# Kernel tuning notes

Measured on AMD Instinct MI355X. Metric: run time of the kernel, lower is better.

Reference implementation:

```python
import jax, jax.numpy as jnp
import numpy as np

R, N, B = 3, 8192, 4096
IN_DIM, HID, OUT = 256, 128, 64
EPS = 1e-5


def _bn(x, g, b):
    # BatchNorm1d in training mode: biased batch stats over dim 0
    m = jnp.mean(x, axis=0)
    v = jnp.var(x, axis=0)
    return (x - m) * jax.lax.rsqrt(v + EPS) * g + b


def setup_inputs() -> dict:
    key = jax.random.key(0)
    k1, k2, k3, k4, k5 = jax.random.split(key, 5)
    features = jax.random.normal(k1, (N, IN_DIM), dtype=jnp.float32)
    u = jax.random.uniform(k2, (R, N, N), dtype=jnp.float32)
    adj = (u < 0.01).astype(jnp.float32)
    batch_nodes = jax.random.randint(k3, (B,), 0, N, dtype=jnp.int32)
    w1 = jax.random.uniform(k4, (IN_DIM, HID), dtype=jnp.float32)  # torch.rand init
    w2 = jax.random.uniform(k5, (HID, OUT), dtype=jnp.float32)
    return {
        "features": features, "adj": adj, "batch_nodes": batch_nodes,
        "w1": w1, "w2": w2,
        "gamma1": jnp.ones((IN_DIM,), jnp.float32), "beta1": jnp.zeros((IN_DIM,), jnp.float32),
        "gamma2": jnp.ones((OUT,), jnp.float32), "beta2": jnp.zeros((OUT,), jnp.float32),
    }


def reference(features, adj, batch_nodes, w1, w2, gamma1, beta1, gamma2, beta2):
    # gather batch subgraph
    x = features[batch_nodes]                       # [B, IN_DIM]
    bA = jnp.take(jnp.take(adj, batch_nodes, axis=1), batch_nodes, axis=2)  # [R, B, B]
    xn = _bn(x, gamma1, beta1)                      # shared across relations

    def per_relation(badj):
        A = badj + jnp.eye(B, dtype=badj.dtype)
        # D_mx.inverse().sqrt() of a diagonal degree matrix == diag(deg^-1/2)
        dinv = jax.lax.rsqrt(jnp.sum(A, axis=1))    # [B]
        A_hat = A * dinv[:, None] * dinv[None, :]   # D^-1/2 A D^-1/2
        h1 = jax.nn.sigmoid(jax.nn.elu((A_hat @ xn) @ w1))   # conv1 + sigmoid
        h2 = jax.nn.elu((A_hat @ h1) @ w2)                   # conv2
        return _bn(h2, gamma2, beta2)

    embed = jax.vmap(per_relation)(bA)              # [R, B, OUT]
    return jax.nn.relu(jnp.mean(embed, axis=0))     # [B, OUT]
```

## Files before the change

### kernel.cpp

```cpp
#include <hip/hip_runtime.h>
#include <hip/hip_bf16.h>

#define RR 3
#define NN 8192
#define BB 4096
#define IN_DIM 256
#define HID 128
#define OUT 64
#define CAPD 128
#define EPS 1e-5f
#define MWN (NN / 64)
#define MLPB 16

__global__ __launch_bounds__(1024) void prep_k(const int* __restrict__ bn,
                                               unsigned long long* __restrict__ memb,
                                               unsigned short* __restrict__ rankg,
                                               unsigned short* __restrict__ nodeof,
                                               float* __restrict__ multf,
                                               int* __restrict__ Ucnt,
                                               unsigned short* __restrict__ pos2slot) {
    __shared__ int smult[NN];
    __shared__ unsigned short srank[NN];
    __shared__ unsigned long long smemb[MWN];
    __shared__ int sbase[MWN + 1];
    int t = threadIdx.x;
    for (int u = t; u < NN; u += 1024) smult[u] = 0;
    __syncthreads();
    for (int i = t; i < BB; i += 1024) atomicAdd(&smult[bn[i]], 1);
    __syncthreads();
    if (t < MWN) {
        unsigned long long w = 0;
        for (int b = 0; b < 64; ++b) if (smult[t * 64 + b]) w |= (1ull << b);
        smemb[t] = w;
        memb[t] = w;
    }
    __syncthreads();
    if (t == 0) {
        int acc = 0;
        for (int m = 0; m < MWN; ++m) { sbase[m] = acc; acc += (int)__popcll(smemb[m]); }
        sbase[MWN] = acc;
        *Ucnt = acc;
    }
    __syncthreads();
    if (t < MWN) {
        unsigned long long w = smemb[t];
        int p = sbase[t];
        while (w) {
            int b = __builtin_ctzll(w); w &= w - 1;
            int u = t * 64 + b;
            srank[u] = (unsigned short)p;
            rankg[u] = (unsigned short)p;
            nodeof[p] = (unsigned short)u;
            multf[p]  = (float)smult[u];
            ++p;
        }
    }
    __syncthreads();
    for (int i = t; i < BB; i += 1024) pos2slot[i] = srank[bn[i]];
}

__global__ __launch_bounds__(256) void bn1_stats_k(const float* __restrict__ feat,
                                                   const int* __restrict__ bn,
                                                   float* __restrict__ m1,
                                                   float* __restrict__ rs1) {
    int c = blockIdx.x;
    float s = 0.f, q = 0.f;
    for (int i = threadIdx.x; i < BB; i += 256) {
        float v = feat[(size_t)bn[i] * IN_DIM + c];
        s += v; q += v * v;
    }
    int lane = threadIdx.x & 63, wv = threadIdx.x >> 6;
    for (int o = 32; o; o >>= 1) { s += __shfl_down(s, o); q += __shfl_down(q, o); }
    __shared__ float ps[4], pq[4];
    if (lane == 0) { ps[wv] = s; pq[wv] = q; }
    __syncthreads();
    if (threadIdx.x == 0) {
        float S = ps[0] + ps[1] + ps[2] + ps[3];
        float Q = pq[0] + pq[1] + pq[2] + pq[3];
        float m = S / BB;
        float v = Q / BB - m * m;
        m1[c] = m;
        rs1[c] = rsqrtf(v + EPS);
    }
}

__global__ __launch_bounds__(256) void xn_c_k(const float* __restrict__ feat,
                                              const unsigned short* __restrict__ nodeof,
                                              const int* __restrict__ Ucnt,
                                              const float* __restrict__ m1,
                                              const float* __restrict__ rs1,
                                              const float* __restrict__ g1,
                                              const float* __restrict__ b1,
                                              float* __restrict__ xn_c) {
    int s = blockIdx.x;
    if (s >= *Ucnt) return;
    int u = nodeof[s];
    int c = threadIdx.x;
    float v = feat[(size_t)u * IN_DIM + c];
    xn_c[(size_t)s * IN_DIM + c] = (v - m1[c]) * rs1[c] * g1[c] + b1[c];
}

__global__ __launch_bounds__(256) void build_k(const float* __restrict__ adj,
                                               const unsigned short* __restrict__ nodeof,
                                               const int* __restrict__ Ucnt,
                                               const unsigned long long* __restrict__ memb,
                                               const unsigned short* __restrict__ rankg,
                                               const float* __restrict__ multf,
                                               unsigned short* __restrict__ cols,
                                               int* __restrict__ cnt,
                                               float* __restrict__ dinv) {
    int blk = blockIdx.x;
    int r = blk >> 12, s = blk & (BB - 1);
    if (s >= *Ucnt) return;
    int u = nodeof[s];
    __shared__ unsigned char nib[2048];
    __shared__ unsigned int rawb[256];
    __shared__ unsigned long long sel[MWN];
    __shared__ int sbase[MWN + 1];
    __shared__ float pdeg[4];
    int t = threadIdx.x;
    const float4* ar4 = (const float4*)(adj + ((size_t)r * NN + u) * NN);
    #pragma unroll
    for (int ch = 0; ch < 8; ++ch) {
        float4 v = ar4[ch * 256 + t];
        nib[ch * 256 + t] = (unsigned char)((v.x != 0.f) | ((v.y != 0.f) << 1) |
                                            ((v.z != 0.f) << 2) | ((v.w != 0.f) << 3));
    }
    __syncthreads();
    {
        unsigned long long x = *(const unsigned long long*)&nib[t * 8];
        x = (x | (x >> 4))  & 0x00FF00FF00FF00FFull;
        x = (x | (x >> 8))  & 0x0000FFFF0000FFFFull;
        x = (x | (x >> 16));
        rawb[t] = (unsigned int)x;
    }
    __syncthreads();
    if (t < MWN) {
        unsigned long long w = ((unsigned long long)rawb[2 * t + 1] << 32) | rawb[2 * t];
        sel[t] = w & memb[t];
    }
    __syncthreads();
    if (t < 64) {
        int p0 = (int)__popcll(sel[2 * t]);
        int p1 = (int)__popcll(sel[2 * t + 1]);
        int x = p0 + p1, xs = x;
        for (int o = 1; o < 64; o <<= 1) { int y = __shfl_up(xs, o); if (t >= o) xs += y; }
        sbase[2 * t]     = xs - x;
        sbase[2 * t + 1] = xs - p1;
        if (t == 63) sbase[MWN] = xs;
    }
    __syncthreads();
    float wdeg = 0.f;
    if (t < MWN) {
        unsigned long long w = sel[t];
        int p = sbase[t];
        unsigned short* cb = cols + (size_t)blk * CAPD;
        while (w) {
            int b = __builtin_ctzll(w); w &= w - 1;
            int v = t * 64 + b;
            int rv = rankg[v];
            if (p < CAPD) cb[p] = (unsigned short)rv;
            wdeg += multf[rv];
            ++p;
        }
    }
    int lane = t & 63, wv = t >> 6;
    for (int o = 32; o; o >>= 1) wdeg += __shfl_down(wdeg, o);
    if (lane == 0) pdeg[wv] = wdeg;
    __syncthreads();
    if (t == 0) {
        int tot = sbase[MWN];
        cnt[blk] = tot < CAPD ? tot : CAPD;
        dinv[blk] = rsqrtf(pdeg[0] + pdeg[1] + pdeg[2] + pdeg[3] + 1.0f);
    }
}

__global__ __launch_bounds__(256) void layer1_agg_k(const float* __restrict__ xn_c,
                                                    const unsigned short* __restrict__ cols,
                                                    const int* __restrict__ cnt,
                                                    const float* __restrict__ dinv,
                                                    const float* __restrict__ multf,
                                                    const int* __restrict__ Ucnt,
                                                    float* __restrict__ y1) {
    int blk = blockIdx.x;
    int r = blk >> 12, s = blk & (BB - 1);
    if (s >= *Ucnt) return;
    int c = threadIdx.x;
    __shared__ unsigned short scl[CAPD];
    __shared__ float swl[CAPD];
    int n = cnt[blk];
    if (c < n) {
        int sl = cols[(size_t)blk * CAPD + c];
        scl[c] = (unsigned short)sl;
        swl[c] = multf[sl] * dinv[(r << 12) + sl];
    }
    __syncthreads();
    float di = dinv[blk];
    float acc = di * xn_c[(size_t)s * IN_DIM + c];
    #pragma unroll 4
    for (int k = 0; k < n; ++k) {
        acc += swl[k] * xn_c[(size_t)scl[k] * IN_DIM + c];
    }
    y1[(size_t)blk * IN_DIM + c] = acc * di;
}

__global__ __launch_bounds__(256) void mlp1_k(const float* __restrict__ y1,
                                              const int* __restrict__ Ucnt,
                                              const float* __restrict__ w1,
                                              float* __restrict__ h1) {
    int blk = blockIdx.x;
    int r = blk / (BB / MLPB), base = (blk % (BB / MLPB)) * MLPB;
    int U = *Ucnt;
    if (base >= U) return;
    int t = threadIdx.x;
    __shared__ float ys[MLPB][IN_DIM];
    #pragma unroll
    for (int s = 0; s < MLPB; ++s) {
        int slot = base + s;
        ys[s][t] = (slot < U) ? y1[((size_t)(r << 12) + slot) * IN_DIM + t] : 0.f;
    }
    __syncthreads();
    int c = t & 127, g = t >> 7;
    float acc[8] = {0.f};
    for (int k = 0; k < IN_DIM; ++k) {
        float wv = w1[k * HID + c];
        #pragma unroll
        for (int j = 0; j < 8; ++j) acc[j] += ys[g * 8 + j][k] * wv;
    }
    #pragma unroll
    for (int j = 0; j < 8; ++j) {
        int slot = base + g * 8 + j;
        if (slot < U) {
            float z = acc[j];
            float e = z > 0.f ? z : expm1f(z);
            h1[((size_t)(r << 12) + slot) * HID + c] = 1.f / (1.f + expf(-e));
        }
    }
}

__global__ __launch_bounds__(128) void layer2_agg_k(const float* __restrict__ h1,
                                                    const unsigned short* __restrict__ cols,
                                                    const int* __restrict__ cnt,
                                                    const float* __restrict__ dinv,
                                                    const float* __restrict__ multf,
                                                    const int* __restrict__ Ucnt,
                                                    float* __restrict__ y2) {
    int blk = blockIdx.x;
    int r = blk >> 12, s = blk & (BB - 1);
    if (s >= *Ucnt) return;
    int c = threadIdx.x;
    __shared__ unsigned short scl[CAPD];
    __shared__ float swl[CAPD];
    int n = cnt[blk];
    if (c < n) {
        int sl = cols[(size_t)blk * CAPD + c];
        scl[c] = (unsigned short)sl;
        swl[c] = multf[sl] * dinv[(r << 12) + sl];
    }
    __syncthreads();
    const float* h1r = h1 + ((size_t)(r << 12)) * HID;
    float di = dinv[blk];
    float acc = di * h1r[(size_t)s * HID + c];
    #pragma unroll 4
    for (int k = 0; k < n; ++k) {
        acc += swl[k] * h1r[(size_t)scl[k] * HID + c];
    }
    y2[(size_t)blk * HID + c] = acc * di;
}

__global__ __launch_bounds__(256) void mlp2_k(const float* __restrict__ y2,
                                              const int* __restrict__ Ucnt,
                                              const float* __restrict__ w2,
                                              float* __restrict__ h2) {
    int blk = blockIdx.x;
    int r = blk / (BB / MLPB), base = (blk % (BB / MLPB)) * MLPB;
    int U = *Ucnt;
    if (base >= U) return;
    int t = threadIdx.x;
    __shared__ float ys[MLPB][HID];
    #pragma unroll
    for (int s = t >> 7; s < MLPB; s += 2) {
        int slot = base + s;
        ys[s][t & 127] = (slot < U) ? y2[((size_t)(r << 12) + slot) * HID + (t & 127)] : 0.f;
    }
    __syncthreads();
    int c = t & 63, g = t >> 6;
    float acc[4] = {0.f};
    for (int k = 0; k < HID; ++k) {
        float wv = w2[k * OUT + c];
        #pragma unroll
        for (int j = 0; j < 4; ++j) acc[j] += ys[g * 4 + j][k] * wv;
    }
    #pragma unroll
    for (int j = 0; j < 4; ++j) {
        int slot = base + g * 4 + j;
        if (slot < U) {
            float z = acc[j];
            h2[((size_t)(r << 12) + slot) * OUT + c] = z > 0.f ? z : expm1f(z);
        }
    }
}

__global__ __launch_bounds__(256) void bn2_stats_k(const float* __restrict__ h2,
                                                   const float* __restrict__ multf,
                                                   const int* __restrict__ Ucnt,
                                                   float* __restrict__ m2,
                                                   float* __restrict__ rs2) {
    int ro = blockIdx.x;
    int r = ro >> 6, o = ro & (OUT - 1);
    int U = *Ucnt;
    float s = 0.f, q = 0.f;
    for (int sl = threadIdx.x; sl < U; sl += 256) {
        float m = multf[sl];
        float v = h2[(size_t)((r << 12) + sl) * OUT + o];
        s += m * v; q += m * v * v;
    }
    int lane = threadIdx.x & 63, wv = threadIdx.x >> 6;
    for (int off = 32; off; off >>= 1) { s += __shfl_down(s, off); q += __shfl_down(q, off); }
    __shared__ float ps[4], pq[4];
    if (lane == 0) { ps[wv] = s; pq[wv] = q; }
    __syncthreads();
    if (threadIdx.x == 0) {
        float S = ps[0] + ps[1] + ps[2] + ps[3];
        float Q = pq[0] + pq[1] + pq[2] + pq[3];
        float m = S / BB;
        float v = Q / BB - m * m;
        m2[ro] = m;
        rs2[ro] = rsqrtf(v + EPS);
    }
}

__global__ __launch_bounds__(256) void finalize_k(const float* __restrict__ h2,
                                                  const unsigned short* __restrict__ pos2slot,
                                                  const float* __restrict__ m2,
                                                  const float* __restrict__ rs2,
                                                  const float* __restrict__ g2,
                                                  const float* __restrict__ b2,
                                                  float* __restrict__ out) {
    int idx = blockIdx.x * 256 + threadIdx.x;
    if (idx >= BB * OUT) return;
    int i = idx >> 6, o = idx & (OUT - 1);
    int sl = pos2slot[i];
    float s = 0.f;
    for (int r = 0; r < RR; ++r) {
        float v = h2[(size_t)((r << 12) + sl) * OUT + o];
        s += (v - m2[r * OUT + o]) * rs2[r * OUT + o] * g2[o] + b2[o];
    }
    s *= (1.0f / RR);
    out[idx] = s > 0.f ? s : 0.f;
}

extern "C" void kernel_launch(void* const* d_in, const int* in_sizes, int n_in,
                              void* d_out, int out_size, void* d_ws, size_t ws_size,
                              hipStream_t stream) {
    const float* feat = (const float*)d_in[0];
    const float* adj  = (const float*)d_in[1];
    const int*   bn   = (const int*)d_in[2];
    const float* w1   = (const float*)d_in[3];
    const float* w2   = (const float*)d_in[4];
    const float* g1   = (const float*)d_in[5];
    const float* b1   = (const float*)d_in[6];
    const float* g2   = (const float*)d_in[7];
    const float* b2   = (const float*)d_in[8];
    float* out = (float*)d_out;

    char* ws = (char*)d_ws;
    size_t off = 0;
    auto alloc = [&](size_t bytes) { size_t o = off; off += (bytes + 255) & ~(size_t)255; return o; };
    unsigned long long* memb = (unsigned long long*)(ws + alloc(MWN * 8));
    unsigned short* rankg    = (unsigned short*)(ws + alloc(NN * 2));
    unsigned short* nodeof   = (unsigned short*)(ws + alloc(BB * 2));
    float* multf             = (float*)(ws + alloc(BB * 4));
    int* Ucnt                = (int*)(ws + alloc(4));
    unsigned short* pos2slot = (unsigned short*)(ws + alloc(BB * 2));
    float* m1                = (float*)(ws + alloc(IN_DIM * 4));
    float* rs1               = (float*)(ws + alloc(IN_DIM * 4));
    float* m2                = (float*)(ws + alloc(RR * OUT * 4));
    float* rs2               = (float*)(ws + alloc(RR * OUT * 4));
    float* xn_c              = (float*)(ws + alloc((size_t)BB * IN_DIM * 4));
    unsigned short* cols     = (unsigned short*)(ws + alloc((size_t)RR * BB * CAPD * 2));
    int* cnt                 = (int*)(ws + alloc((size_t)RR * BB * 4));
    float* dinv              = (float*)(ws + alloc((size_t)RR * BB * 4));
    float* y1                = (float*)(ws + alloc((size_t)RR * BB * IN_DIM * 4));
    float* h1                = (float*)(ws + alloc((size_t)RR * BB * HID * 4));
    float* y2                = (float*)(ws + alloc((size_t)RR * BB * HID * 4));
    float* h2                = (float*)(ws + alloc((size_t)RR * BB * OUT * 4));

    prep_k<<<1, 1024, 0, stream>>>(bn, memb, rankg, nodeof, multf, Ucnt, pos2slot);
    bn1_stats_k<<<IN_DIM, 256, 0, stream>>>(feat, bn, m1, rs1);
    xn_c_k<<<BB, 256, 0, stream>>>(feat, nodeof, Ucnt, m1, rs1, g1, b1, xn_c);
    build_k<<<RR * BB, 256, 0, stream>>>(adj, nodeof, Ucnt, memb, rankg, multf, cols, cnt, dinv);
    layer1_agg_k<<<RR * BB, 256, 0, stream>>>(xn_c, cols, cnt, dinv, multf, Ucnt, y1);
    mlp1_k<<<RR * (BB / MLPB), 256, 0, stream>>>(y1, Ucnt, w1, h1);
    layer2_agg_k<<<RR * BB, 128, 0, stream>>>(h1, cols, cnt, dinv, multf, Ucnt, y2);
    mlp2_k<<<RR * (BB / MLPB), 256, 0, stream>>>(y2, Ucnt, w2, h2);
    bn2_stats_k<<<RR * OUT, 256, 0, stream>>>(h2, multf, Ucnt, m2, rs2);
    finalize_k<<<(BB * OUT + 255) / 256, 256, 0, stream>>>(h2, pos2slot, m2, rs2, g2, b2, out);
}
```

Measured before the change: 172.1 us.

## Fold BN1 affine into layer-1 aggregation and merge prep with BN1 stats

The BN1 statistics and the membership prep move into one launch, with the prep work done by a single extra block alongside the per-channel stats blocks. The normalized feature buffer and its kernel are removed. Layer-1 aggregation now gathers raw features by node id and applies the BN affine algebraically, using the summed edge weights to scale the bias term. To support this, the column list stores both slot rank and node id packed into 32-bit entries. This saves one launch and one intermediate write/read, at the cost of doubling the cols footprint and reading scattered rows of the larger features array.

```diff
diff --git a/kernel.cpp b/kernel.cpp
--- a/kernel.cpp
+++ b/kernel.cpp
@@ -12,21 +12,49 @@
 #define MWN (NN / 64)
 #define MLPB 16
 
-__global__ __launch_bounds__(1024) void prep_k(const int* __restrict__ bn,
-                                               unsigned long long* __restrict__ memb,
-                                               unsigned short* __restrict__ rankg,
-                                               unsigned short* __restrict__ nodeof,
-                                               float* __restrict__ multf,
-                                               int* __restrict__ Ucnt,
-                                               unsigned short* __restrict__ pos2slot) {
+__global__ __launch_bounds__(256) void k1_bn1_prep_k(const float* __restrict__ feat,
+                                                     const int* __restrict__ bn,
+                                                     const float* __restrict__ g1,
+                                                     const float* __restrict__ b1,
+                                                     float* __restrict__ af,
+                                                     float* __restrict__ bfv,
+                                                     unsigned long long* __restrict__ memb,
+                                                     unsigned short* __restrict__ rankg,
+                                                     unsigned short* __restrict__ nodeof,
+                                                     float* __restrict__ multf,
+                                                     int* __restrict__ Ucnt,
+                                                     unsigned short* __restrict__ pos2slot) {
     __shared__ int smult[NN];
     __shared__ unsigned short srank[NN];
     __shared__ unsigned long long smemb[MWN];
     __shared__ int sbase[MWN + 1];
+    __shared__ float ps[4], pq[4];
     int t = threadIdx.x;
-    for (int u = t; u < NN; u += 1024) smult[u] = 0;
-    __syncthreads();
-    for (int i = t; i < BB; i += 1024) atomicAdd(&smult[bn[i]], 1);
+    if (blockIdx.x < IN_DIM) {
+        int c = blockIdx.x;
+        float s = 0.f, q = 0.f;
+        for (int i = t; i < BB; i += 256) {
+            float v = feat[(size_t)bn[i] * IN_DIM + c];
+            s += v; q += v * v;
+        }
+        int lane = t & 63, wv = t >> 6;
+        for (int o = 32; o; o >>= 1) { s += __shfl_down(s, o); q += __shfl_down(q, o); }
+        if (lane == 0) { ps[wv] = s; pq[wv] = q; }
+        __syncthreads();
+        if (t == 0) {
+            float S = ps[0] + ps[1] + ps[2] + ps[3];
+            float Q = pq[0] + pq[1] + pq[2] + pq[3];
+            float m = S / BB;
+            float rs = rsqrtf(Q / BB - m * m + EPS);
+            float a = rs * g1[c];
+            af[c]  = a;
+            bfv[c] = b1[c] - m * a;
+        }
+        return;
+    }
+    for (int u = t; u < NN; u += 256) smult[u] = 0;
+    __syncthreads();
+    for (int i = t; i < BB; i += 256) atomicAdd(&smult[bn[i]], 1);
     __syncthreads();
     if (t < MWN) {
         unsigned long long w = 0;
@@ -56,48 +84,7 @@
         }
     }
     __syncthreads();
-    for (int i = t; i < BB; i += 1024) pos2slot[i] = srank[bn[i]];
-}
-
-__global__ __launch_bounds__(256) void bn1_stats_k(const float* __restrict__ feat,
-                                                   const int* __restrict__ bn,
-                                                   float* __restrict__ m1,
-                                                   float* __restrict__ rs1) {
-    int c = blockIdx.x;
-    float s = 0.f, q = 0.f;
-    for (int i = threadIdx.x; i < BB; i += 256) {
-        float v = feat[(size_t)bn[i] * IN_DIM + c];
-        s += v; q += v * v;
-    }
-    int lane = threadIdx.x & 63, wv = threadIdx.x >> 6;
-    for (int o = 32; o; o >>= 1) { s += __shfl_down(s, o); q += __shfl_down(q, o); }
-    __shared__ float ps[4], pq[4];
-    if (lane == 0) { ps[wv] = s; pq[wv] = q; }
-    __syncthreads();
-    if (threadIdx.x == 0) {
-        float S = ps[0] + ps[1] + ps[2] + ps[3];
-        float Q = pq[0] + pq[1] + pq[2] + pq[3];
-        float m = S / BB;
-        float v = Q / BB - m * m;
-        m1[c] = m;
-        rs1[c] = rsqrtf(v + EPS);
-    }
-}
-
-__global__ __launch_bounds__(256) void xn_c_k(const float* __restrict__ feat,
-                                              const unsigned short* __restrict__ nodeof,
-                                              const int* __restrict__ Ucnt,
-                                              const float* __restrict__ m1,
-                                              const float* __restrict__ rs1,
-                                              const float* __restrict__ g1,
-                                              const float* __restrict__ b1,
-                                              float* __restrict__ xn_c) {
-    int s = blockIdx.x;
-    if (s >= *Ucnt) return;
-    int u = nodeof[s];
-    int c = threadIdx.x;
-    float v = feat[(size_t)u * IN_DIM + c];
-    xn_c[(size_t)s * IN_DIM + c] = (v - m1[c]) * rs1[c] * g1[c] + b1[c];
+    for (int i = t; i < BB; i += 256) pos2slot[i] = srank[bn[i]];
 }
 
 __global__ __launch_bounds__(256) void build_k(const float* __restrict__ adj,
@@ -106,7 +93,7 @@
                                                const unsigned long long* __restrict__ memb,
                                                const unsigned short* __restrict__ rankg,
                                                const float* __restrict__ multf,
-                                               unsigned short* __restrict__ cols,
+                                               unsigned* __restrict__ cols,
                                                int* __restrict__ cnt,
                                                float* __restrict__ dinv) {
     int blk = blockIdx.x;
@@ -154,12 +141,12 @@
     if (t < MWN) {
         unsigned long long w = sel[t];
         int p = sbase[t];
-        unsigned short* cb = cols + (size_t)blk * CAPD;
+        unsigned* cb = cols + (size_t)blk * CAPD;
         while (w) {
             int b = __builtin_ctzll(w); w &= w - 1;
             int v = t * 64 + b;
             int rv = rankg[v];
-            if (p < CAPD) cb[p] = (unsigned short)rv;
+            if (p < CAPD) cb[p] = ((unsigned)rv << 13) | (unsigned)v;
             wdeg += multf[rv];
             ++p;
         }
@@ -175,13 +162,85 @@
     }
 }
 
-__global__ __launch_bounds__(256) void layer1_agg_k(const float* __restrict__ xn_c,
-                                                    const unsigned short* __restrict__ cols,
-                                                    const int* __restrict__ cnt,
-                                                    const float* __restrict__ dinv,
-                                                    const float* __restrict__ multf,
-                                                    const int* __restrict__ Ucnt,
-                                                    float* __restrict__ y1) {
+__global__ __launch_bounds__(256) void agg1_k(const float* __restrict__ feat,
+                                              const unsigned* __restrict__ cols,
+                                              const int* __restrict__ cnt,
+                                              const float* __restrict__ dinv,
+                                              const float* __restrict__ multf,
+                                              const unsigned short* __restrict__ nodeof,
+                                              const int* __restrict__ Ucnt,
+                                              const float* __restrict__ af,
+                                              const float* __restrict__ bfv,
+                                              float* __restrict__ y1) {
+    int blk = blockIdx.x;
+    int r = blk >> 12, s = blk & (BB - 1);
+    if (s >= *Ucnt) return;
+    int c = threadIdx.x;
+    __shared__ unsigned short snode[CAPD];
+    __shared__ float swl[CAPD];
+    int n = cnt[blk];
+    if (c < n) {
+        unsigned e = cols[(size_t)blk * CAPD + c];
+        int sl = e >> 13;
+        snode[c] = (unsigned short)(e & 8191u);
+        swl[c] = multf[sl] * dinv[(r << 12) + sl];
+    }
+    __syncthreads();
+    float di = dinv[blk];
+    float acc = di * feat[(size_t)nodeof[s] * IN_DIM + c];
+    float sw = 0.f;
+    #pragma unroll 4
+    for (int k = 0; k < n; ++k) {
+        float w = swl[k];
+        sw += w;
+        acc += w * feat[(size_t)snode[k] * IN_DIM + c];
+    }
+    float raw = acc * di;
+    float f = di * (di + sw);
+    y1[(size_t)blk * IN_DIM + c] = af[c] * raw + bfv[c] * f;
+}
+
+__global__ __launch_bounds__(256) void mlp1_k(const float* __restrict__ y1,
+                                              const int* __restrict__ Ucnt,
+                                              const float* __restrict__ w1,
+                                              float* __restrict__ h1) {
+    int blk = blockIdx.x;
+    int r = blk / (BB / MLPB), base = (blk % (BB / MLPB)) * MLPB;
+    int U = *Ucnt;
+    if (base >= U) return;
+    int t = threadIdx.x;
+    __shared__ float ys[MLPB][IN_DIM];
+    #pragma unroll
+    for (int s = 0; s < MLPB; ++s) {
+        int slot = base + s;
+        ys[s][t] = (slot < U) ? y1[((size_t)(r << 12) + slot) * IN_DIM + t] : 0.f;
+    }
+    __syncthreads();
+    int c = t & 127, g = t >> 7;
+    float acc[8] = {0.f};
+    for (int k = 0; k < IN_DIM; ++k) {
+        float wv = w1[k * HID + c];
+        #pragma unroll
+        for (int j = 0; j < 8; ++j) acc[j] += ys[g * 8 + j][k] * wv;
+    }
+    #pragma unroll
+    for (int j = 0; j < 8; ++j) {
+        int slot = base + g * 8 + j;
+        if (slot < U) {
+            float z = acc[j];
+            float e = z > 0.f ? z : expm1f(z);
+            h1[((size_t)(r << 12) + slot) * HID + c] = 1.f / (1.f + expf(-e));
+        }
+    }
+}
+
+__global__ __launch_bounds__(128) void agg2_k(const float* __restrict__ h1,
+                                              const unsigned* __restrict__ cols,
+                                              const int* __restrict__ cnt,
+                                              const float* __restrict__ dinv,
+                                              const float* __restrict__ multf,
+                                              const int* __restrict__ Ucnt,
+                                              float* __restrict__ y2) {
     int blk = blockIdx.x;
     int r = blk >> 12, s = blk & (BB - 1);
     if (s >= *Ucnt) return;
@@ -190,70 +249,8 @@
     __shared__ float swl[CAPD];
     int n = cnt[blk];
     if (c < n) {
-        int sl = cols[(size_t)blk * CAPD + c];
-        scl[c] = (unsigned short)sl;
-        swl[c] = multf[sl] * dinv[(r << 12) + sl];
-    }
-    __syncthreads();
-    float di = dinv[blk];
-    float acc = di * xn_c[(size_t)s * IN_DIM + c];
-    #pragma unroll 4
-    for (int k = 0; k < n; ++k) {
-        acc += swl[k] * xn_c[(size_t)scl[k] * IN_DIM + c];
-    }
-    y1[(size_t)blk * IN_DIM + c] = acc * di;
-}
-
-__global__ __launch_bounds__(256) void mlp1_k(const float* __restrict__ y1,
-                                              const int* __restrict__ Ucnt,
-                                              const float* __restrict__ w1,
-                                              float* __restrict__ h1) {
-    int blk = blockIdx.x;
-    int r = blk / (BB / MLPB), base = (blk % (BB / MLPB)) * MLPB;
-    int U = *Ucnt;
-    if (base >= U) return;
-    int t = threadIdx.x;
-    __shared__ float ys[MLPB][IN_DIM];
-    #pragma unroll
-    for (int s = 0; s < MLPB; ++s) {
-        int slot = base + s;
-        ys[s][t] = (slot < U) ? y1[((size_t)(r << 12) + slot) * IN_DIM + t] : 0.f;
-    }
-    __syncthreads();
-    int c = t & 127, g = t >> 7;
-    float acc[8] = {0.f};
-    for (int k = 0; k < IN_DIM; ++k) {
-        float wv = w1[k * HID + c];
-        #pragma unroll
-        for (int j = 0; j < 8; ++j) acc[j] += ys[g * 8 + j][k] * wv;
-    }
-    #pragma unroll
-    for (int j = 0; j < 8; ++j) {
-        int slot = base + g * 8 + j;
-        if (slot < U) {
-            float z = acc[j];
-            float e = z > 0.f ? z : expm1f(z);
-            h1[((size_t)(r << 12) + slot) * HID + c] = 1.f / (1.f + expf(-e));
-        }
-    }
-}
-
-__global__ __launch_bounds__(128) void layer2_agg_k(const float* __restrict__ h1,
-                                                    const unsigned short* __restrict__ cols,
-                                                    const int* __restrict__ cnt,
-                                                    const float* __restrict__ dinv,
-                                                    const float* __restrict__ multf,
-                                                    const int* __restrict__ Ucnt,
-                                                    float* __restrict__ y2) {
-    int blk = blockIdx.x;
-    int r = blk >> 12, s = blk & (BB - 1);
-    if (s >= *Ucnt) return;
-    int c = threadIdx.x;
-    __shared__ unsigned short scl[CAPD];
-    __shared__ float swl[CAPD];
-    int n = cnt[blk];
-    if (c < n) {
-        int sl = cols[(size_t)blk * CAPD + c];
+        unsigned e = cols[(size_t)blk * CAPD + c];
+        int sl = e >> 13;
         scl[c] = (unsigned short)sl;
         swl[c] = multf[sl] * dinv[(r << 12) + sl];
     }
@@ -373,12 +370,11 @@
     float* multf             = (float*)(ws + alloc(BB * 4));
     int* Ucnt                = (int*)(ws + alloc(4));
     unsigned short* pos2slot = (unsigned short*)(ws + alloc(BB * 2));
-    float* m1                = (float*)(ws + alloc(IN_DIM * 4));
-    float* rs1               = (float*)(ws + alloc(IN_DIM * 4));
+    float* af                = (float*)(ws + alloc(IN_DIM * 4));
+    float* bfv               = (float*)(ws + alloc(IN_DIM * 4));
     float* m2                = (float*)(ws + alloc(RR * OUT * 4));
     float* rs2               = (float*)(ws + alloc(RR * OUT * 4));
-    float* xn_c              = (float*)(ws + alloc((size_t)BB * IN_DIM * 4));
-    unsigned short* cols     = (unsigned short*)(ws + alloc((size_t)RR * BB * CAPD * 2));
+    unsigned* cols           = (unsigned*)(ws + alloc((size_t)RR * BB * CAPD * 4));
     int* cnt                 = (int*)(ws + alloc((size_t)RR * BB * 4));
     float* dinv              = (float*)(ws + alloc((size_t)RR * BB * 4));
     float* y1                = (float*)(ws + alloc((size_t)RR * BB * IN_DIM * 4));
@@ -386,13 +382,12 @@
     float* y2                = (float*)(ws + alloc((size_t)RR * BB * HID * 4));
     float* h2                = (float*)(ws + alloc((size_t)RR * BB * OUT * 4));
 
-    prep_k<<<1, 1024, 0, stream>>>(bn, memb, rankg, nodeof, multf, Ucnt, pos2slot);
-    bn1_stats_k<<<IN_DIM, 256, 0, stream>>>(feat, bn, m1, rs1);
-    xn_c_k<<<BB, 256, 0, stream>>>(feat, nodeof, Ucnt, m1, rs1, g1, b1, xn_c);
+    k1_bn1_prep_k<<<IN_DIM + 1, 256, 0, stream>>>(feat, bn, g1, b1, af, bfv,
+                                                  memb, rankg, nodeof, multf, Ucnt, pos2slot);
     build_k<<<RR * BB, 256, 0, stream>>>(adj, nodeof, Ucnt, memb, rankg, multf, cols, cnt, dinv);
-    layer1_agg_k<<<RR * BB, 256, 0, stream>>>(xn_c, cols, cnt, dinv, multf, Ucnt, y1);
+    agg1_k<<<RR * BB, 256, 0, stream>>>(feat, cols, cnt, dinv, multf, nodeof, Ucnt, af, bfv, y1);
     mlp1_k<<<RR * (BB / MLPB), 256, 0, stream>>>(y1, Ucnt, w1, h1);
-    layer2_agg_k<<<RR * BB, 128, 0, stream>>>(h1, cols, cnt, dinv, multf, Ucnt, y2);
+    agg2_k<<<RR * BB, 128, 0, stream>>>(h1, cols, cnt, dinv, multf, Ucnt, y2);
     mlp2_k<<<RR * (BB / MLPB), 256, 0, stream>>>(y2, Ucnt, w2, h2);
     bn2_stats_k<<<RR * OUT, 256, 0, stream>>>(h2, multf, Ucnt, m2, rs2);
     finalize_k<<<(BB * OUT + 255) / 256, 256, 0, stream>>>(h2, pos2slot, m2, rs2, g2, b2, out);
```

After: 164.9 us. 4.2% less time.
